# Performance work log

Measured on AMD Instinct MI355X. Metric: run time of the kernel, lower is better.

## Reference

```python
import jax, jax.numpy as jnp
import numpy as np

IN_DIMS, CELL_DIMS, OUT_DIMS, T = 64, 128, 64, 256
BATCH = 4096


def _xavier(key, shape):
    fan_in, fan_out = shape
    limit = float(np.sqrt(6.0 / (fan_in + fan_out)))
    return jax.random.uniform(key, shape, jnp.float32, -limit, limit)


def setup_inputs() -> dict:
    key = jax.random.key(0)
    k_in, k_k, k_rk, k_b, k_dw, k_db = jax.random.split(key, 6)
    inputs = jax.random.normal(k_in, (BATCH, T, IN_DIMS), jnp.float32)
    kernel = _xavier(k_k, (IN_DIMS, 2 * CELL_DIMS))
    recurrent_kernel = _xavier(k_rk, (CELL_DIMS, 2 * CELL_DIMS))
    # bias: forget-gate half initialized to log(1 + (T-2)*U[0,1)), rest zeros
    u = jax.random.uniform(k_b, (CELL_DIMS,), jnp.float32)
    recurrent_bias = jnp.concatenate(
        [jnp.log(1.0 + (T - 1 - 1.0) * u), jnp.zeros((CELL_DIMS,), jnp.float32)])
    # nn.Linear(cell_dims, out_dims): uniform(-1/sqrt(cell), 1/sqrt(cell))
    bound = 1.0 / float(np.sqrt(CELL_DIMS))
    dense_w = jax.random.uniform(k_dw, (CELL_DIMS, OUT_DIMS), jnp.float32, -bound, bound)
    dense_b = jax.random.uniform(k_db, (OUT_DIMS,), jnp.float32, -bound, bound)
    return {"inputs": inputs, "kernel": kernel, "recurrent_kernel": recurrent_kernel,
            "recurrent_bias": recurrent_bias, "dense_w": dense_w, "dense_b": dense_b}


def reference(inputs, kernel, recurrent_kernel, recurrent_bias, dense_w, dense_b):
    B = inputs.shape[0]
    cell = recurrent_kernel.shape[0]
    # Precompute input projections for all timesteps: [B, T, 2*cell]
    zx = jnp.einsum('bti,ic->btc', inputs, kernel) + recurrent_bias

    def step(c_state, zx_t):
        z = zx_t + c_state @ recurrent_kernel  # h_state == c_state
        f = jax.nn.sigmoid(z[:, :cell])
        c = f * c_state + (1.0 - f) * jnp.tanh(z[:, cell:])
        return c, None

    c0 = jnp.zeros((B, cell), inputs.dtype)
    h_final, _ = jax.lax.scan(step, c0, jnp.swapaxes(zx, 0, 1))  # scan over T
    return h_final @ dense_w + dense_b
```

## Files before the change

kernel.cpp:

```cpp
#include <hip/hip_runtime.h>

#define BATCH 4096
#define T 256
#define IN 64
#define CELL 128
#define ZDIM 256
#define OUTD 64
#define M 16

using f32x4 = __attribute__((ext_vector_type(4))) float;
using f4    = __attribute__((ext_vector_type(4))) float;
using h16x8 = __attribute__((ext_vector_type(8))) _Float16;
using fp16x2 = __attribute__((ext_vector_type(2))) __fp16;
typedef unsigned int u32t;

union h8cast { h16x8 v; fp16x2 h[4]; };

#define GATE(FA, FB, GA, GB, CREG, WO)                                          \
    _Pragma("unroll") for (int i = 0; i < 4; ++i) {                             \
      float zf = FA[i] + FB[i];                                                 \
      float zg = GA[i] + GB[i];                                                 \
      float fg = __builtin_amdgcn_rcpf(1.f + __expf(-zf));                      \
      float th = 1.f - 2.f * __builtin_amdgcn_rcpf(__expf(2.f * zg) + 1.f);     \
      float cn = fg * (CREG[i] - th) + th;                                      \
      CREG[i] = cn;                                                             \
      *(_Float16*)(cn_ + WO[i]) = (_Float16)cn;                                 \
    }

#define STEP(XC0, XC1, XC2, XC3, TT, P)                                         \
  {                                                                             \
    const char* cb_ = cbuf[P];                                                  \
    h16x8 ca0 = *(const h16x8*)(cb_ + ro[0]);                                   \
    h16x8 ca1 = *(const h16x8*)(cb_ + ro[1]);                                   \
    h16x8 ca2 = *(const h16x8*)(cb_ + ro[2]);                                   \
    h16x8 ca3 = *(const h16x8*)(cb_ + ro[3]);                                   \
    h8cast ux0, ux1;                                                            \
    ux0.h[0] = __builtin_amdgcn_cvt_pkrtz(XC0[0], XC0[1]);                      \
    ux0.h[1] = __builtin_amdgcn_cvt_pkrtz(XC0[2], XC0[3]);                      \
    ux0.h[2] = __builtin_amdgcn_cvt_pkrtz(XC1[0], XC1[1]);                      \
    ux0.h[3] = __builtin_amdgcn_cvt_pkrtz(XC1[2], XC1[3]);                      \
    ux1.h[0] = __builtin_amdgcn_cvt_pkrtz(XC2[0], XC2[1]);                      \
    ux1.h[1] = __builtin_amdgcn_cvt_pkrtz(XC2[2], XC2[3]);                      \
    ux1.h[2] = __builtin_amdgcn_cvt_pkrtz(XC3[0], XC3[1]);                      \
    ux1.h[3] = __builtin_amdgcn_cvt_pkrtz(XC3[2], XC3[3]);                      \
    const h16x8 xa0 = ux0.v, xa1 = ux1.v;                                       \
    {                                                                           \
      const int tn = (TT) + 2 < T ? (TT) + 2 : T - 1;                           \
      const float* xp = xrow + (size_t)tn * IN;                                 \
      XC0 = *(const f4*)(xp + 8 * g);                                           \
      XC1 = *(const f4*)(xp + 8 * g + 4);                                       \
      XC2 = *(const f4*)(xp + 32 + 8 * g);                                      \
      XC3 = *(const f4*)(xp + 32 + 8 * g + 4);                                  \
    }                                                                           \
                            \
    f32x4 fa0 = __builtin_amdgcn_mfma_f32_16x16x32_f16(xa0, bA0, bqA, 0, 0, 0); \
    f32x4 fb0 = __builtin_amdgcn_mfma_f32_16x16x32_f16(xa0, bB0, bqB, 0, 0, 0); \
    f32x4 ga0 = __builtin_amdgcn_mfma_f32_16x16x32_f16(xa0, bC0, bqC, 0, 0, 0); \
    f32x4 gb0 = __builtin_amdgcn_mfma_f32_16x16x32_f16(xa0, bD0, bqD, 0, 0, 0); \
    f32x4 fa1 = __builtin_amdgcn_mfma_f32_16x16x32_f16(xa1, bA1, zq, 0, 0, 0);  \
    f32x4 fb1 = __builtin_amdgcn_mfma_f32_16x16x32_f16(xa1, bB1, zq, 0, 0, 0);  \
    f32x4 ga1 = __builtin_amdgcn_mfma_f32_16x16x32_f16(xa1, bC1, zq, 0, 0, 0);  \
    f32x4 gb1 = __builtin_amdgcn_mfma_f32_16x16x32_f16(xa1, bD1, zq, 0, 0, 0);  \
    fa0 = __builtin_amdgcn_mfma_f32_16x16x32_f16(ca0, bA2, fa0, 0, 0, 0);       \
    fb0 = __builtin_amdgcn_mfma_f32_16x16x32_f16(ca0, bB2, fb0, 0, 0, 0);       \
    ga0 = __builtin_amdgcn_mfma_f32_16x16x32_f16(ca0, bC2, ga0, 0, 0, 0);       \
    gb0 = __builtin_amdgcn_mfma_f32_16x16x32_f16(ca0, bD2, gb0, 0, 0, 0);       \
    fa1 = __builtin_amdgcn_mfma_f32_16x16x32_f16(ca1, bA3, fa1, 0, 0, 0);       \
    fb1 = __builtin_amdgcn_mfma_f32_16x16x32_f16(ca1, bB3, fb1, 0, 0, 0);       \
    ga1 = __builtin_amdgcn_mfma_f32_16x16x32_f16(ca1, bC3, ga1, 0, 0, 0);       \
    gb1 = __builtin_amdgcn_mfma_f32_16x16x32_f16(ca1, bD3, gb1, 0, 0, 0);       \
    fa0 = __builtin_amdgcn_mfma_f32_16x16x32_f16(ca2, bA4, fa0, 0, 0, 0);       \
    fb0 = __builtin_amdgcn_mfma_f32_16x16x32_f16(ca2, bB4, fb0, 0, 0, 0);       \
    ga0 = __builtin_amdgcn_mfma_f32_16x16x32_f16(ca2, bC4, ga0, 0, 0, 0);       \
    gb0 = __builtin_amdgcn_mfma_f32_16x16x32_f16(ca2, bD4, gb0, 0, 0, 0);       \
    fa1 = __builtin_amdgcn_mfma_f32_16x16x32_f16(ca3, bA5, fa1, 0, 0, 0);       \
    fb1 = __builtin_amdgcn_mfma_f32_16x16x32_f16(ca3, bB5, fb1, 0, 0, 0);       \
    ga1 = __builtin_amdgcn_mfma_f32_16x16x32_f16(ca3, bC5, ga1, 0, 0, 0);       \
    gb1 = __builtin_amdgcn_mfma_f32_16x16x32_f16(ca3, bD5, gb1, 0, 0, 0);       \
    char* cn_ = cbuf[(P) ^ 1];                                                  \
    GATE(fa0, fa1, ga0, ga1, cregA, woA)                                        \
    GATE(fb0, fb1, gb0, gb1, cregB, woB)                                        \
      \
    asm volatile("s_waitcnt lgkmcnt(0)\n\ts_barrier" ::: "memory");             \
  }

__global__ __launch_bounds__(256, 1)
void llrnn_f16(const float* __restrict__ in,
               const float* __restrict__ Km,
               const float* __restrict__ Rm,
               const float* __restrict__ bz,
               const float* __restrict__ Wd,
               const float* __restrict__ bd,
               float* __restrict__ out)
{
  __shared__ __align__(16) char cbuf[2][M * CELL * 2];
  __shared__ float cfin[M * CELL];

  const int tid = threadIdx.x;
  const int w = tid >> 6;
  const int l = tid & 63;
  const int q = l & 15;
  const int g = l >> 4;
  const int rb = blockIdx.x * M;
  const int jA = 32 * w + q;
  const int jB = 32 * w + 16 + q;

  {
    u32t* z0 = (u32t*)cbuf[0];
    z0[tid] = 0; z0[tid + 256] = 0; z0[tid + 512] = 0; z0[tid + 768] = 0;
  }

  h16x8 bA0,bA1,bA2,bA3,bA4,bA5, bB0,bB1,bB2,bB3,bB4,bB5,
        bC0,bC1,bC2,bC3,bC4,bC5, bD0,bD1,bD2,bD3,bD4,bD5;
#define LOADW(DST, COL, KT)                                                     \
  {                                                                             \
    _Pragma("unroll") for (int e = 0; e < 8; ++e) {                             \
      const int krow = 32 * (KT) + 8 * g + e;                                   \
      const float* src = ((KT) < 2) ? (Km + (size_t)krow * ZDIM)                \
                                    : (Rm + (size_t)(krow - IN) * ZDIM);        \
      DST[e] = (_Float16)src[COL];                                              \
    }                                                                           \
  }
  LOADW(bA0,jA,0) LOADW(bA1,jA,1) LOADW(bA2,jA,2) LOADW(bA3,jA,3) LOADW(bA4,jA,4) LOADW(bA5,jA,5)
  LOADW(bB0,jB,0) LOADW(bB1,jB,1) LOADW(bB2,jB,2) LOADW(bB3,jB,3) LOADW(bB4,jB,4) LOADW(bB5,jB,5)
  LOADW(bC0,jA+CELL,0) LOADW(bC1,jA+CELL,1) LOADW(bC2,jA+CELL,2) LOADW(bC3,jA+CELL,3) LOADW(bC4,jA+CELL,4) LOADW(bC5,jA+CELL,5)
  LOADW(bD0,jB+CELL,0) LOADW(bD1,jB+CELL,1) LOADW(bD2,jB+CELL,2) LOADW(bD3,jB+CELL,3) LOADW(bD4,jB+CELL,4) LOADW(bD5,jB+CELL,5)
#undef LOADW
  f32x4 zq = {0.f, 0.f, 0.f, 0.f};
  asm volatile("" : "+v"(bA0),"+v"(bA1),"+v"(bA2),"+v"(bA3),"+v"(bA4),"+v"(bA5),
                    "+v"(bB0),"+v"(bB1),"+v"(bB2),"+v"(bB3),"+v"(bB4),"+v"(bB5),
                    "+v"(bC0),"+v"(bC1),"+v"(bC2),"+v"(bC3),"+v"(bC4),"+v"(bC5),
                    "+v"(bD0),"+v"(bD1),"+v"(bD2),"+v"(bD3),"+v"(bD4),"+v"(bD5),
                    "+v"(zq));

  const float bA_ = bz[jA], bB_ = bz[jB], bC_ = bz[jA + CELL], bD_ = bz[jB + CELL];
  const f32x4 bqA = {bA_, bA_, bA_, bA_};
  const f32x4 bqB = {bB_, bB_, bB_, bB_};
  const f32x4 bqC = {bC_, bC_, bC_, bC_};
  const f32x4 bqD = {bD_, bD_, bD_, bD_};

  int ro[4];
#pragma unroll
  for (int ct = 0; ct < 4; ++ct)
    ro[ct] = q * 256 + 16 * ((4 * ct + g) ^ (q & 7));
  int woA[4], woB[4];
#pragma unroll
  for (int i = 0; i < 4; ++i) {
    const int r = 4 * g + i;
    woA[i] = r * 256 + 16 * ((4 * w + (q >> 3)) ^ (r & 7)) + ((2 * q) & 15);
    woB[i] = r * 256 + 16 * ((4 * w + 2 + (q >> 3)) ^ (r & 7)) + ((2 * q) & 15);
  }

  const float* xrow = in + (size_t)(rb + q) * T * IN;
  f4 xc0 = *(const f4*)(xrow + 8 * g);
  f4 xc1 = *(const f4*)(xrow + 8 * g + 4);
  f4 xc2 = *(const f4*)(xrow + 32 + 8 * g);
  f4 xc3 = *(const f4*)(xrow + 32 + 8 * g + 4);
  f4 xn0 = *(const f4*)(xrow + IN + 8 * g);
  f4 xn1 = *(const f4*)(xrow + IN + 8 * g + 4);
  f4 xn2 = *(const f4*)(xrow + IN + 32 + 8 * g);
  f4 xn3 = *(const f4*)(xrow + IN + 32 + 8 * g + 4);

  f32x4 cregA = {0.f, 0.f, 0.f, 0.f};
  f32x4 cregB = {0.f, 0.f, 0.f, 0.f};

  __syncthreads();

  for (int t = 0; t < T; t += 2) {
    STEP(xc0, xc1, xc2, xc3, t, 0)
    STEP(xn0, xn1, xn2, xn3, t + 1, 1)
  }

#pragma unroll
  for (int i = 0; i < 4; ++i) {
    cfin[(4 * g + i) * CELL + jA] = cregA[i];
    cfin[(4 * g + i) * CELL + jB] = cregB[i];
  }
  __syncthreads();

  const int o = tid & 63;
  const int rp = tid >> 6;
  float a0 = bd[o], a1 = bd[o], a2 = bd[o], a3 = bd[o];
#pragma unroll 4
  for (int k = 0; k < CELL; ++k) {
    const float wv = Wd[(size_t)k * OUTD + o];
    a0 += cfin[rp * CELL + k] * wv;
    a1 += cfin[(rp + 4) * CELL + k] * wv;
    a2 += cfin[(rp + 8) * CELL + k] * wv;
    a3 += cfin[(rp + 12) * CELL + k] * wv;
  }
  out[(size_t)(rb + rp) * OUTD + o] = a0;
  out[(size_t)(rb + rp + 4) * OUTD + o] = a1;
  out[(size_t)(rb + rp + 8) * OUTD + o] = a2;
  out[(size_t)(rb + rp + 12) * OUTD + o] = a3;
}

extern "C" void kernel_launch(void* const* d_in, const int* in_sizes, int n_in,
                              void* d_out, int out_size, void* d_ws, size_t ws_size,
                              hipStream_t stream) {
  const float* in  = (const float*)d_in[0];
  const float* Km  = (const float*)d_in[1];
  const float* Rm  = (const float*)d_in[2];
  const float* bz  = (const float*)d_in[3];
  const float* Wd  = (const float*)d_in[4];
  const float* bd  = (const float*)d_in[5];
  float* out = (float*)d_out;

  dim3 grid(BATCH / M);
  dim3 block(256);
  hipLaunchKernelGGL(llrnn_f16, grid, block, 0, stream,
                     in, Km, Rm, bz, Wd, bd, out);
}
```

Before: 171.0 us.

## Prescale weights for exp2 gates, pack paired-column state stores, pin weights in AGPRs

Folds the sigmoid and tanh exponent scaling (-log2e and 2*log2e) into the fp16 weights and biases at load time, so the gates use the raw exp2 instruction with no multiply. Each lane now owns adjacent column pairs (2q, 2q+1) instead of q and q+16, so the two new state values are packed into one 32-bit LDS store rather than two 16-bit stores. The weight fragments are pinned to AGPRs instead of VGPRs, and the x-prefetch address math is simplified to a mask-based wrap. Scaling the weights before rounding to fp16 slightly changes the rounding error, and the new write-offset swizzle has to stay consistent with the read layout.

Result: slower. 180.0 us (+5.2%).

```diff
diff --git a/kernel.cpp b/kernel.cpp
--- a/kernel.cpp
+++ b/kernel.cpp
@@ -15,17 +15,22 @@
 typedef unsigned int u32t;
 
 union h8cast { h16x8 v; fp16x2 h[4]; };
-
-#define GATE(FA, FB, GA, GB, CREG, WO)                                          \
-    _Pragma("unroll") for (int i = 0; i < 4; ++i) {                             \
-      float zf = FA[i] + FB[i];                                                 \
-      float zg = GA[i] + GB[i];                                                 \
-      float fg = __builtin_amdgcn_rcpf(1.f + __expf(-zf));                      \
-      float th = 1.f - 2.f * __builtin_amdgcn_rcpf(__expf(2.f * zg) + 1.f);     \
-      float cn = fg * (CREG[i] - th) + th;                                      \
-      CREG[i] = cn;                                                             \
-      *(_Float16*)(cn_ + WO[i]) = (_Float16)cn;                                 \
-    }
+union pkcast { fp16x2 h; u32t u; };
+
+#define GATEPK(I)                                                               \
+  {                                                                             \
+    float zfA = fa0[I] + fa1[I], zgA = ga0[I] + ga1[I];                         \
+    float zfB = fb0[I] + fb1[I], zgB = gb0[I] + gb1[I];                         \
+    float fgA = __builtin_amdgcn_rcpf(1.f + __builtin_amdgcn_exp2f(zfA));       \
+    float thA = 1.f - 2.f * __builtin_amdgcn_rcpf(__builtin_amdgcn_exp2f(zgA) + 1.f); \
+    float cnA = fgA * (cregA[I] - thA) + thA;                                   \
+    float fgB = __builtin_amdgcn_rcpf(1.f + __builtin_amdgcn_exp2f(zfB));       \
+    float thB = 1.f - 2.f * __builtin_amdgcn_rcpf(__builtin_amdgcn_exp2f(zgB) + 1.f); \
+    float cnB = fgB * (cregB[I] - thB) + thB;                                   \
+    cregA[I] = cnA; cregB[I] = cnB;                                             \
+    pkcast pk_; pk_.h = __builtin_amdgcn_cvt_pkrtz(cnA, cnB);                   \
+    *(u32t*)(cn_ + woPk[I]) = pk_.u;                                            \
+  }
 
 #define STEP(XC0, XC1, XC2, XC3, TT, P)                                         \
   {                                                                             \
@@ -44,15 +49,16 @@
     ux1.h[2] = __builtin_amdgcn_cvt_pkrtz(XC3[0], XC3[1]);                      \
     ux1.h[3] = __builtin_amdgcn_cvt_pkrtz(XC3[2], XC3[3]);                      \
     const h16x8 xa0 = ux0.v, xa1 = ux1.v;                                       \
+                  \
     {                                                                           \
-      const int tn = (TT) + 2 < T ? (TT) + 2 : T - 1;                           \
-      const float* xp = xrow + (size_t)tn * IN;                                 \
-      XC0 = *(const f4*)(xp + 8 * g);                                           \
-      XC1 = *(const f4*)(xp + 8 * g + 4);                                       \
-      XC2 = *(const f4*)(xp + 32 + 8 * g);                                      \
-      XC3 = *(const f4*)(xp + 32 + 8 * g + 4);                                  \
+      const int tn = ((TT) + 2) & (T - 1);                                      \
+      const float* xp = xbase + (size_t)tn * IN;                                \
+      XC0 = *(const f4*)(xp);                                                   \
+      XC1 = *(const f4*)(xp + 4);                                               \
+      XC2 = *(const f4*)(xp + 32);                                              \
+      XC3 = *(const f4*)(xp + 36);                                              \
     }                                                                           \
-                            \
+                                            \
     f32x4 fa0 = __builtin_amdgcn_mfma_f32_16x16x32_f16(xa0, bA0, bqA, 0, 0, 0); \
     f32x4 fb0 = __builtin_amdgcn_mfma_f32_16x16x32_f16(xa0, bB0, bqB, 0, 0, 0); \
     f32x4 ga0 = __builtin_amdgcn_mfma_f32_16x16x32_f16(xa0, bC0, bqC, 0, 0, 0); \
@@ -78,8 +84,7 @@
     ga1 = __builtin_amdgcn_mfma_f32_16x16x32_f16(ca3, bC5, ga1, 0, 0, 0);       \
     gb1 = __builtin_amdgcn_mfma_f32_16x16x32_f16(ca3, bD5, gb1, 0, 0, 0);       \
     char* cn_ = cbuf[(P) ^ 1];                                                  \
-    GATE(fa0, fa1, ga0, ga1, cregA, woA)                                        \
-    GATE(fb0, fb1, gb0, gb1, cregB, woB)                                        \
+    GATEPK(0) GATEPK(1) GATEPK(2) GATEPK(3)                                     \
       \
     asm volatile("s_waitcnt lgkmcnt(0)\n\ts_barrier" ::: "memory");             \
   }
@@ -102,64 +107,71 @@
   const int q = l & 15;
   const int g = l >> 4;
   const int rb = blockIdx.x * M;
-  const int jA = 32 * w + q;
-  const int jB = 32 * w + 16 + q;
+  const int colA = 32 * w + 2 * q;
+  const int colB = colA + 1;
 
   {
     u32t* z0 = (u32t*)cbuf[0];
     z0[tid] = 0; z0[tid + 256] = 0; z0[tid + 512] = 0; z0[tid + 768] = 0;
   }
 
+  const float SF = -1.44269504f;
+  const float SG =  2.88539008f;
+
   h16x8 bA0,bA1,bA2,bA3,bA4,bA5, bB0,bB1,bB2,bB3,bB4,bB5,
         bC0,bC1,bC2,bC3,bC4,bC5, bD0,bD1,bD2,bD3,bD4,bD5;
-#define LOADW(DST, COL, KT)                                                     \
+#define LOADW(DST, COL, KT, SC)                                                 \
   {                                                                             \
     _Pragma("unroll") for (int e = 0; e < 8; ++e) {                             \
       const int krow = 32 * (KT) + 8 * g + e;                                   \
       const float* src = ((KT) < 2) ? (Km + (size_t)krow * ZDIM)                \
                                     : (Rm + (size_t)(krow - IN) * ZDIM);        \
-      DST[e] = (_Float16)src[COL];                                              \
+      DST[e] = (_Float16)(src[COL] * (SC));                                     \
     }                                                                           \
   }
-  LOADW(bA0,jA,0) LOADW(bA1,jA,1) LOADW(bA2,jA,2) LOADW(bA3,jA,3) LOADW(bA4,jA,4) LOADW(bA5,jA,5)
-  LOADW(bB0,jB,0) LOADW(bB1,jB,1) LOADW(bB2,jB,2) LOADW(bB3,jB,3) LOADW(bB4,jB,4) LOADW(bB5,jB,5)
-  LOADW(bC0,jA+CELL,0) LOADW(bC1,jA+CELL,1) LOADW(bC2,jA+CELL,2) LOADW(bC3,jA+CELL,3) LOADW(bC4,jA+CELL,4) LOADW(bC5,jA+CELL,5)
-  LOADW(bD0,jB+CELL,0) LOADW(bD1,jB+CELL,1) LOADW(bD2,jB+CELL,2) LOADW(bD3,jB+CELL,3) LOADW(bD4,jB+CELL,4) LOADW(bD5,jB+CELL,5)
+  LOADW(bA0,colA,0,SF) LOADW(bA1,colA,1,SF) LOADW(bA2,colA,2,SF)
+  LOADW(bA3,colA,3,SF) LOADW(bA4,colA,4,SF) LOADW(bA5,colA,5,SF)
+  LOADW(bB0,colB,0,SF) LOADW(bB1,colB,1,SF) LOADW(bB2,colB,2,SF)
+  LOADW(bB3,colB,3,SF) LOADW(bB4,colB,4,SF) LOADW(bB5,colB,5,SF)
+  LOADW(bC0,colA+CELL,0,SG) LOADW(bC1,colA+CELL,1,SG) LOADW(bC2,colA+CELL,2,SG)
+  LOADW(bC3,colA+CELL,3,SG) LOADW(bC4,colA+CELL,4,SG) LOADW(bC5,colA+CELL,5,SG)
+  LOADW(bD0,colB+CELL,0,SG) LOADW(bD1,colB+CELL,1,SG) LOADW(bD2,colB+CELL,2,SG)
+  LOADW(bD3,colB+CELL,3,SG) LOADW(bD4,colB+CELL,4,SG) LOADW(bD5,colB+CELL,5,SG)
 #undef LOADW
-  f32x4 zq = {0.f, 0.f, 0.f, 0.f};
-  asm volatile("" : "+v"(bA0),"+v"(bA1),"+v"(bA2),"+v"(bA3),"+v"(bA4),"+v"(bA5),
-                    "+v"(bB0),"+v"(bB1),"+v"(bB2),"+v"(bB3),"+v"(bB4),"+v"(bB5),
-                    "+v"(bC0),"+v"(bC1),"+v"(bC2),"+v"(bC3),"+v"(bC4),"+v"(bC5),
-                    "+v"(bD0),"+v"(bD1),"+v"(bD2),"+v"(bD3),"+v"(bD4),"+v"(bD5),
-                    "+v"(zq));
-
-  const float bA_ = bz[jA], bB_ = bz[jB], bC_ = bz[jA + CELL], bD_ = bz[jB + CELL];
-  const f32x4 bqA = {bA_, bA_, bA_, bA_};
-  const f32x4 bqB = {bB_, bB_, bB_, bB_};
-  const f32x4 bqC = {bC_, bC_, bC_, bC_};
-  const f32x4 bqD = {bD_, bD_, bD_, bD_};
+  asm volatile("" : "+a"(bA0),"+a"(bA1),"+a"(bA2),"+a"(bA3),"+a"(bA4),"+a"(bA5),
+                    "+a"(bB0),"+a"(bB1),"+a"(bB2),"+a"(bB3),"+a"(bB4),"+a"(bB5),
+                    "+a"(bC0),"+a"(bC1),"+a"(bC2),"+a"(bC3),"+a"(bC4),"+a"(bC5),
+                    "+a"(bD0),"+a"(bD1),"+a"(bD2),"+a"(bD3),"+a"(bD4),"+a"(bD5));
+
+  const float bA_ = bz[colA] * SF, bB_ = bz[colB] * SF;
+  const float bC_ = bz[colA + CELL] * SG, bD_ = bz[colB + CELL] * SG;
+  f32x4 bqA = {bA_, bA_, bA_, bA_};
+  f32x4 bqB = {bB_, bB_, bB_, bB_};
+  f32x4 bqC = {bC_, bC_, bC_, bC_};
+  f32x4 bqD = {bD_, bD_, bD_, bD_};
+  f32x4 zq  = {0.f, 0.f, 0.f, 0.f};
+  asm volatile("" : "+v"(bqA), "+v"(bqB), "+v"(bqC), "+v"(bqD), "+v"(zq));
 
   int ro[4];
 #pragma unroll
   for (int ct = 0; ct < 4; ++ct)
     ro[ct] = q * 256 + 16 * ((4 * ct + g) ^ (q & 7));
-  int woA[4], woB[4];
+  int woPk[4];
 #pragma unroll
   for (int i = 0; i < 4; ++i) {
     const int r = 4 * g + i;
-    woA[i] = r * 256 + 16 * ((4 * w + (q >> 3)) ^ (r & 7)) + ((2 * q) & 15);
-    woB[i] = r * 256 + 16 * ((4 * w + 2 + (q >> 3)) ^ (r & 7)) + ((2 * q) & 15);
-  }
-
-  const float* xrow = in + (size_t)(rb + q) * T * IN;
-  f4 xc0 = *(const f4*)(xrow + 8 * g);
-  f4 xc1 = *(const f4*)(xrow + 8 * g + 4);
-  f4 xc2 = *(const f4*)(xrow + 32 + 8 * g);
-  f4 xc3 = *(const f4*)(xrow + 32 + 8 * g + 4);
-  f4 xn0 = *(const f4*)(xrow + IN + 8 * g);
-  f4 xn1 = *(const f4*)(xrow + IN + 8 * g + 4);
-  f4 xn2 = *(const f4*)(xrow + IN + 32 + 8 * g);
-  f4 xn3 = *(const f4*)(xrow + IN + 32 + 8 * g + 4);
+    woPk[i] = r * 256 + 16 * ((4 * w + (q >> 2)) ^ (r & 7)) + ((4 * q) & 15);
+  }
+
+  const float* xbase = in + (size_t)(rb + q) * T * IN + 8 * g;
+  f4 xc0 = *(const f4*)(xbase);
+  f4 xc1 = *(const f4*)(xbase + 4);
+  f4 xc2 = *(const f4*)(xbase + 32);
+  f4 xc3 = *(const f4*)(xbase + 36);
+  f4 xn0 = *(const f4*)(xbase + 64);
+  f4 xn1 = *(const f4*)(xbase + 68);
+  f4 xn2 = *(const f4*)(xbase + 96);
+  f4 xn3 = *(const f4*)(xbase + 100);
 
   f32x4 cregA = {0.f, 0.f, 0.f, 0.f};
   f32x4 cregB = {0.f, 0.f, 0.f, 0.f};
@@ -173,8 +185,8 @@
 
 #pragma unroll
   for (int i = 0; i < 4; ++i) {
-    cfin[(4 * g + i) * CELL + jA] = cregA[i];
-    cfin[(4 * g + i) * CELL + jB] = cregB[i];
+    cfin[(4 * g + i) * CELL + colA] = cregA[i];
+    cfin[(4 * g + i) * CELL + colB] = cregB[i];
   }
   __syncthreads();
 
```
